# Optimization experiments

Measured on AMD Instinct MI355X. Metric: run time of the kernel, lower is better.

## Reference

```python
import jax, jax.numpy as jnp
import numpy as np

OBJECTNESS_LIMIT = 0.7
NUM_ANCHORS = 9
DN = ('NHWC', 'HWIO', 'NHWC')


def _conv(x, w, b):
    return jax.lax.conv_general_dilated(x, w, (1, 1), 'SAME', dimension_numbers=DN) + b


def setup_inputs() -> dict:
    key = jax.random.key(0)
    ks = jax.random.split(key, 4)
    B, H, W, Cin = 4, 256, 256, 64
    x = jax.random.normal(ks[0], (B, H, W, Cin), dtype=jnp.float32)
    # base: Conv2D(512, 3x3, relu, kernel_initializer='normal')
    w_base = jax.random.normal(ks[1], (3, 3, Cin, 512), dtype=jnp.float32) * 0.02
    b_base = jnp.zeros((512,), dtype=jnp.float32)
    # classifier: Conv2D(9, 1x1, sigmoid, kernel_initializer='uniform')
    w_cls = jax.random.uniform(ks[2], (1, 1, 512, NUM_ANCHORS), dtype=jnp.float32, minval=-0.05, maxval=0.05)
    b_cls = jnp.zeros((NUM_ANCHORS,), dtype=jnp.float32)
    w_reg = jax.random.normal(ks[3], (1, 1, 512, 4 * NUM_ANCHORS), dtype=jnp.float32) * 0.02
    b_reg = jnp.zeros((4 * NUM_ANCHORS,), dtype=jnp.float32)
    return {"x": x, "w_base": w_base, "b_base": b_base,
            "w_cls": w_cls, "b_cls": b_cls, "w_reg": w_reg, "b_reg": b_reg}


def reference(x, w_base, b_base, w_cls, b_cls, w_reg, b_reg):
    # shared 3x3 conv trunk
    feat = jax.nn.relu(_conv(x, w_base, b_base))                 # [B,H,W,512]
    # per-anchor objectness
    scores = jax.nn.sigmoid(_conv(feat, w_cls, b_cls))           # [B,H,W,A]
    deltas = _conv(feat, w_reg, b_reg)                           # [B,H,W,4A]
    B, H, W, A = scores.shape
    # vectorized form of the per-anchor threshold loop: keep deltas only
    # where objectness > limit (gather/filter expressed as a mask)
    mask = (scores > OBJECTNESS_LIMIT).astype(deltas.dtype)      # [B,H,W,A]
    masked = (deltas.reshape(B, H, W, A, 4) * mask[..., None]).reshape(B, H, W, 4 * A)
    return jnp.concatenate([scores, masked], axis=-1)            # [B,H,W,5A]
```

## Files before the change

kernel.cpp:

```cpp
#include <hip/hip_runtime.h>
#include <hip/hip_bf16.h>
#include <math.h>


typedef _Float16 fp16x8 __attribute__((ext_vector_type(8)));
typedef _Float16 fp16x4 __attribute__((ext_vector_type(4)));
typedef float    f32x4  __attribute__((ext_vector_type(4)));

#define BT_ELEMS  (18 * 32 * 64 * 8)
#define BT2_ELEMS (48 * 512)
#define BS_BYTES  32768

__global__ __launch_bounds__(256) void rpn_prep(
    const float* __restrict__ wb,
    const float* __restrict__ wc,
    const float* __restrict__ wr,
    _Float16* __restrict__ btI,
    _Float16* __restrict__ bt2_hi, _Float16* __restrict__ bt2_lo)
{
    int t = blockIdx.x * 256 + threadIdx.x;
    if (t < BT_ELEMS) {
        int e    = t & 7;
        int lane = (t >> 3) & 63;
        int j    = (t >> 9) & 31;
        int s    = t >> 14;
        int wv   = j >> 3, l = j & 7;
        int lr   = lane & 15, q = lane >> 4;
        int n    = wv * 128 + l * 16 + lr;
        int k    = s * 32 + q * 8 + e;
        int tap  = k >> 6, c = k & 63;
        btI[t] = (_Float16)wb[(tap * 64 + c) * 512 + n];
    } else if (t < BT_ELEMS + BT2_ELEMS) {
        int jj = t - BT_ELEMS;
        int k = jj & 511;
        int o = jj >> 9;
        float v = 0.f;
        if (o < 9)       v = wc[k * 9 + o];
        else if (o < 45) v = wr[k * 36 + (o - 9)];
        _Float16 h = (_Float16)v;
        bt2_hi[jj] = h;
        bt2_lo[jj] = (_Float16)(v - (float)h);
    }
}

#define XS_STRIDE   76
#define FB_OFF      10944
#define FB_PER_WAVE 4608
#define ZB_SLICE    1600
#define ARENA_BYTES 29376

#define LOAD_AH(S, AH)                                                        \
    {                                                                         \
        const int tap_ = (S) >> 1;                                            \
        const int ky_  = tap_ / 3;                                            \
        const int kx_  = tap_ - ky_ * 3;                                      \
        const int c0_  = ((S) & 1) * 32 + q * 8;                              \
        _Pragma("unroll")                                                     \
        for (int km = 0; km < 2; ++km)                                        \
            AH[km] = *(const fp16x8*)&xs_hi[((km + ky_) * 18 + lr + kx_) * XS_STRIDE + c0_]; \
    }

#define MFMA_STEP(AH, BREG)                                                   \
    {                                                                         \
        __builtin_amdgcn_s_setprio(1);                                        \
        _Pragma("unroll")                                                     \
        for (int l = 0; l < 8; ++l) {                                         \
            acc[0][l] = __builtin_amdgcn_mfma_f32_16x16x32_f16(AH[0], BREG[l], acc[0][l], 0, 0, 0); \
            acc[1][l] = __builtin_amdgcn_mfma_f32_16x16x32_f16(AH[1], BREG[l], acc[1][l], 0, 0, 0); \
        }                                                                     \
        __builtin_amdgcn_s_setprio(0);                                        \
    }

__global__ __launch_bounds__(256, 3) void rpn_main(
    const float* __restrict__ x,
    const float* __restrict__ b_base,
    const float* __restrict__ b_cls,
    const float* __restrict__ b_reg,
    const _Float16* __restrict__ btI,
    const _Float16* __restrict__ bt2_hi, const _Float16* __restrict__ bt2_lo,
    float* __restrict__ out)
{
    __shared__ char smem[ARENA_BYTES];
    _Float16* xs_hi = (_Float16*)smem;
    float*    zb    = (float*)smem;

    const int tid  = threadIdx.x;
    const int wave = tid >> 6;
    const int lane = tid & 63;
    const int q    = lane >> 4;
    const int lr   = lane & 15;
    const int n0   = wave * 128;

    const int wg  = blockIdx.x;
    const int b   = wg >> 11;
    const int rem = wg & 2047;
    const int h0  = (rem >> 4) * 2;
    const int w0  = (rem & 15) * 16;

    for (int i = 0; i < 5; ++i) {
        int flat = tid + i * 256;
        if (flat < 4 * 18 * 16) {
            int cq  = flat & 15;
            int rp  = flat >> 4;
            int row = rp / 18;
            int pos = rp - row * 18;
            int hh  = h0 - 1 + row;
            int ww  = w0 - 1 + pos;
            fp16x4 h4;
            if (hh >= 0 && hh < 256 && ww >= 0 && ww < 256) {
                const float4 v = *(const float4*)&x[(((b * 256 + hh) * 256 + ww) * 64 + cq * 4)];
                h4[0] = (_Float16)v.x; h4[1] = (_Float16)v.y;
                h4[2] = (_Float16)v.z; h4[3] = (_Float16)v.w;
            } else {
                #pragma unroll
                for (int j = 0; j < 4; ++j) h4[j] = (_Float16)0.f;
            }
            *(fp16x4*)&xs_hi[(row * 18 + pos) * XS_STRIDE + cq * 4] = h4;
        }
    }

    const char* gW = (const char*)btI + wave * 8192 + lane * 16;

    fp16x8 bA[8], bB[8];
    #pragma unroll
    for (int l = 0; l < 8; ++l)
        bA[l] = *(const fp16x8*)(gW + (size_t)l * 1024);

    __syncthreads();

    f32x4 acc[2][8];
    #pragma unroll
    for (int km = 0; km < 2; ++km)
        #pragma unroll
        for (int l = 0; l < 8; ++l)
            acc[km][l] = (f32x4){0.f, 0.f, 0.f, 0.f};

    fp16x8 ahA[2], ahB[2];
    LOAD_AH(0, ahA);

    #pragma unroll
    for (int s = 0; s < 18; s += 2) {
        {
            const char* g1 = gW + (size_t)(s + 1) * BS_BYTES;
            #pragma unroll
            for (int l = 0; l < 8; ++l)
                bB[l] = *(const fp16x8*)(g1 + (size_t)l * 1024);
        }
        LOAD_AH(s + 1, ahB);
        MFMA_STEP(ahA, bA);
        if (s + 2 < 18) {
            const char* g2 = gW + (size_t)(s + 2) * BS_BYTES;
            #pragma unroll
            for (int l = 0; l < 8; ++l)
                bA[l] = *(const fp16x8*)(g2 + (size_t)l * 1024);
            LOAD_AH(s + 2, ahA);
        }
        MFMA_STEP(ahB, bB);
    }


    _Float16* fh = (_Float16*)(smem + FB_OFF + wave * FB_PER_WAVE);
    _Float16* fl = fh + 32 * 36;

    f32x4 acc2[2][3];
    #pragma unroll
    for (int km = 0; km < 2; ++km)
        #pragma unroll
        for (int ns = 0; ns < 3; ++ns)
            acc2[km][ns] = (f32x4){0.f, 0.f, 0.f, 0.f};

    fp16x8 cwh0, cwl0, cwh1, cwh2;
    {
        const int kg0 = n0 + q * 8;
        cwh0 = *(const fp16x8*)&bt2_hi[(0 * 16 + lr) * 512 + kg0];
        cwl0 = *(const fp16x8*)&bt2_lo[(0 * 16 + lr) * 512 + kg0];
        cwh1 = *(const fp16x8*)&bt2_hi[(1 * 16 + lr) * 512 + kg0];
        cwh2 = *(const fp16x8*)&bt2_hi[(2 * 16 + lr) * 512 + kg0];
    }

    #pragma unroll
    for (int sub = 0; sub < 4; ++sub) {
        #pragma unroll
        for (int lh = 0; lh < 2; ++lh) {
            int l = sub * 2 + lh;
            float bias = b_base[n0 + l * 16 + lr];
            #pragma unroll
            for (int km = 0; km < 2; ++km) {
                #pragma unroll
                for (int r = 0; r < 4; ++r) {
                    float v = acc[km][l][r] + bias;
                    v = v > 0.f ? v : 0.f;
                    _Float16 h = (_Float16)v;
                    int row = km * 16 + q * 4 + r;
                    int col = lh * 16 + lr;
                    fh[row * 36 + col] = h;
                    fl[row * 36 + col] = (_Float16)(v - (float)h);
                }
            }
        }

        fp16x8 nwh0, nwl0, nwh1, nwh2;
        if (sub < 3) {
            const int kgn = n0 + (sub + 1) * 32 + q * 8;
            nwh0 = *(const fp16x8*)&bt2_hi[(0 * 16 + lr) * 512 + kgn];
            nwl0 = *(const fp16x8*)&bt2_lo[(0 * 16 + lr) * 512 + kgn];
            nwh1 = *(const fp16x8*)&bt2_hi[(1 * 16 + lr) * 512 + kgn];
            nwh2 = *(const fp16x8*)&bt2_hi[(2 * 16 + lr) * 512 + kgn];
        }

        asm volatile("s_waitcnt lgkmcnt(0)" ::: "memory");

        fp16x8 fah[2], fal[2];
        #pragma unroll
        for (int km = 0; km < 2; ++km) {
            int off = (km * 16 + lr) * 36 + q * 8;
            union { fp16x8 v8; fp16x4 v4[2]; } uh, ul;
            uh.v4[0] = *(const fp16x4*)&fh[off];
            uh.v4[1] = *(const fp16x4*)&fh[off + 4];
            ul.v4[0] = *(const fp16x4*)&fl[off];
            ul.v4[1] = *(const fp16x4*)&fl[off + 4];
            fah[km] = uh.v8;
            fal[km] = ul.v8;
        }

        __builtin_amdgcn_s_setprio(1);
        #pragma unroll
        for (int km = 0; km < 2; ++km)
            acc2[km][0] = __builtin_amdgcn_mfma_f32_16x16x32_f16(fah[km], cwh0, acc2[km][0], 0, 0, 0);
        #pragma unroll
        for (int km = 0; km < 2; ++km)
            acc2[km][0] = __builtin_amdgcn_mfma_f32_16x16x32_f16(fah[km], cwl0, acc2[km][0], 0, 0, 0);
        #pragma unroll
        for (int km = 0; km < 2; ++km)
            acc2[km][0] = __builtin_amdgcn_mfma_f32_16x16x32_f16(fal[km], cwh0, acc2[km][0], 0, 0, 0);
        #pragma unroll
        for (int km = 0; km < 2; ++km)
            acc2[km][1] = __builtin_amdgcn_mfma_f32_16x16x32_f16(fah[km], cwh1, acc2[km][1], 0, 0, 0);
        #pragma unroll
        for (int km = 0; km < 2; ++km)
            acc2[km][1] = __builtin_amdgcn_mfma_f32_16x16x32_f16(fal[km], cwh1, acc2[km][1], 0, 0, 0);
        #pragma unroll
        for (int km = 0; km < 2; ++km)
            acc2[km][2] = __builtin_amdgcn_mfma_f32_16x16x32_f16(fah[km], cwh2, acc2[km][2], 0, 0, 0);
        #pragma unroll
        for (int km = 0; km < 2; ++km)
            acc2[km][2] = __builtin_amdgcn_mfma_f32_16x16x32_f16(fal[km], cwh2, acc2[km][2], 0, 0, 0);
        __builtin_amdgcn_s_setprio(0);

        if (sub < 3) { cwh0 = nwh0; cwl0 = nwl0; cwh1 = nwh1; cwh2 = nwh2; }
    }

    __syncthreads();

    {
        float* zw = zb + wave * ZB_SLICE;
        #pragma unroll
        for (int km = 0; km < 2; ++km)
            #pragma unroll
            for (int ns = 0; ns < 3; ++ns)
                #pragma unroll
                for (int r = 0; r < 4; ++r) {
                    int row = km * 16 + q * 4 + r;
                    int col = ns * 16 + lr;
                    zw[row * 50 + col] = acc2[km][ns][r];
                }
    }
    __syncthreads();

    for (int i = tid; i < 32 * 45; i += 256) {
        int m = i / 45;
        int o = i - m * 45;
        int e0 = m * 50 + o;
        float z = ((zb[e0] + zb[ZB_SLICE + e0]) + zb[2 * ZB_SLICE + e0]) + zb[3 * ZB_SLICE + e0];
        float v;
        if (o < 9) {
            v = 1.f / (1.f + expf(-(z + b_cls[o])));
        } else {
            int d = o - 9;
            int a = d >> 2;
            int ea = m * 50 + a;
            float za = ((zb[ea] + zb[ZB_SLICE + ea]) + zb[2 * ZB_SLICE + ea]) + zb[3 * ZB_SLICE + ea];
            float s = 1.f / (1.f + expf(-(za + b_cls[a])));
            v = (s > 0.7f) ? (z + b_reg[d]) : 0.f;
        }
        int mh = m >> 4, mw = m & 15;
        out[(((b * 256 + h0 + mh) * 256) + w0 + mw) * 45 + o] = v;
    }
}

extern "C" void kernel_launch(void* const* d_in, const int* in_sizes, int n_in,
                              void* d_out, int out_size, void* d_ws, size_t ws_size,
                              hipStream_t stream)
{
    const float* x      = (const float*)d_in[0];
    const float* w_base = (const float*)d_in[1];
    const float* b_base = (const float*)d_in[2];
    const float* w_cls  = (const float*)d_in[3];
    const float* b_cls  = (const float*)d_in[4];
    const float* w_reg  = (const float*)d_in[5];
    const float* b_reg  = (const float*)d_in[6];
    float* out = (float*)d_out;

    _Float16* btI    = (_Float16*)d_ws;
    _Float16* bt2_hi = btI + BT_ELEMS;
    _Float16* bt2_lo = bt2_hi + BT2_ELEMS;

    rpn_prep<<<(BT_ELEMS + BT2_ELEMS + 255) / 256, 256, 0, stream>>>(
        w_base, w_cls, w_reg, btI, bt2_hi, bt2_lo);
    rpn_main<<<8192, 256, 0, stream>>>(
        x, b_base, b_cls, b_reg, btI, bt2_hi, bt2_lo, out);
}
```

Baseline: 346.9 us.

## Switch trunk conv MFMA from 16x16x32 to 32x32x16 tiles

Replaces the sixteen 16x16x32 MFMAs per K-step with eight 32x32x16 MFMAs covering the same 32x128 output tile per wave. The weight prep kernel re-packs the B operand into the 32x32 operand layout, the A fragments from LDS are reloaded to match, and the epilogue remaps the 16-element accumulators back to row/column positions. The aim is fewer MFMA issues and operand register reads per FLOP. The risk is that the remapped layouts or LDS access patterns create bank conflicts or pipeline stalls.

After: 368.8 us. 1.06x slower.

```diff
diff --git a/kernel.cpp b/kernel.cpp
--- a/kernel.cpp
+++ b/kernel.cpp
@@ -6,6 +6,7 @@
 typedef _Float16 fp16x8 __attribute__((ext_vector_type(8)));
 typedef _Float16 fp16x4 __attribute__((ext_vector_type(4)));
 typedef float    f32x4  __attribute__((ext_vector_type(4)));
+typedef float    f32x16 __attribute__((ext_vector_type(16)));
 
 #define BT_ELEMS  (18 * 32 * 64 * 8)
 #define BT2_ELEMS (48 * 512)
@@ -22,12 +23,12 @@
     if (t < BT_ELEMS) {
         int e    = t & 7;
         int lane = (t >> 3) & 63;
-        int j    = (t >> 9) & 31;
+        int j    = (t >> 9) & 3;
+        int h    = (t >> 11) & 1;
+        int wv   = (t >> 12) & 3;
         int s    = t >> 14;
-        int wv   = j >> 3, l = j & 7;
-        int lr   = lane & 15, q = lane >> 4;
-        int n    = wv * 128 + l * 16 + lr;
-        int k    = s * 32 + q * 8 + e;
+        int n    = wv * 128 + j * 32 + (lane & 31);
+        int k    = s * 32 + h * 16 + ((lane >> 5) << 3) + e;
         int tap  = k >> 6, c = k & 63;
         btI[t] = (_Float16)wb[(tap * 64 + c) * 512 + n];
     } else if (t < BT_ELEMS + BT2_ELEMS) {
@@ -54,20 +55,21 @@
         const int tap_ = (S) >> 1;                                            \
         const int ky_  = tap_ / 3;                                            \
         const int kx_  = tap_ - ky_ * 3;                                      \
-        const int c0_  = ((S) & 1) * 32 + q * 8;                              \
         _Pragma("unroll")                                                     \
-        for (int km = 0; km < 2; ++km)                                        \
-            AH[km] = *(const fp16x8*)&xs_hi[((km + ky_) * 18 + lr + kx_) * XS_STRIDE + c0_]; \
+        for (int h = 0; h < 2; ++h)                                           \
+            AH[h] = *(const fp16x8*)&xs_hi[((hp + ky_) * 18 + lr + kx_) * XS_STRIDE \
+                                           + ((S) & 1) * 32 + h * 16 + l5 * 8]; \
     }
 
 #define MFMA_STEP(AH, BREG)                                                   \
     {                                                                         \
         __builtin_amdgcn_s_setprio(1);                                        \
         _Pragma("unroll")                                                     \
-        for (int l = 0; l < 8; ++l) {                                         \
-            acc[0][l] = __builtin_amdgcn_mfma_f32_16x16x32_f16(AH[0], BREG[l], acc[0][l], 0, 0, 0); \
-            acc[1][l] = __builtin_amdgcn_mfma_f32_16x16x32_f16(AH[1], BREG[l], acc[1][l], 0, 0, 0); \
-        }                                                                     \
+        for (int j = 0; j < 4; ++j)                                           \
+            acc32[j] = __builtin_amdgcn_mfma_f32_32x32x16_f16(AH[0], BREG[j], acc32[j], 0, 0, 0); \
+        _Pragma("unroll")                                                     \
+        for (int j = 0; j < 4; ++j)                                           \
+            acc32[j] = __builtin_amdgcn_mfma_f32_32x32x16_f16(AH[1], BREG[4 + j], acc32[j], 0, 0, 0); \
         __builtin_amdgcn_s_setprio(0);                                        \
     }
 
@@ -89,6 +91,9 @@
     const int lane = tid & 63;
     const int q    = lane >> 4;
     const int lr   = lane & 15;
+    const int l5   = lane >> 5;
+    const int hp   = (lane >> 4) & 1;
+    const int l31  = lane & 31;
     const int n0   = wave * 128;
 
     const int wg  = blockIdx.x;
@@ -113,7 +118,7 @@
                 h4[2] = (_Float16)v.z; h4[3] = (_Float16)v.w;
             } else {
                 #pragma unroll
-                for (int j = 0; j < 4; ++j) h4[j] = (_Float16)0.f;
+                for (int jz = 0; jz < 4; ++jz) h4[jz] = (_Float16)0.f;
             }
             *(fp16x4*)&xs_hi[(row * 18 + pos) * XS_STRIDE + cq * 4] = h4;
         }
@@ -128,12 +133,12 @@
 
     __syncthreads();
 
-    f32x4 acc[2][8];
-    #pragma unroll
-    for (int km = 0; km < 2; ++km)
-        #pragma unroll
-        for (int l = 0; l < 8; ++l)
-            acc[km][l] = (f32x4){0.f, 0.f, 0.f, 0.f};
+    f32x16 acc32[4];
+    #pragma unroll
+    for (int j = 0; j < 4; ++j)
+        #pragma unroll
+        for (int r = 0; r < 16; ++r)
+            acc32[j][r] = 0.f;
 
     fp16x8 ahA[2], ahB[2];
     LOAD_AH(0, ahA);
@@ -180,22 +185,16 @@
 
     #pragma unroll
     for (int sub = 0; sub < 4; ++sub) {
-        #pragma unroll
-        for (int lh = 0; lh < 2; ++lh) {
-            int l = sub * 2 + lh;
-            float bias = b_base[n0 + l * 16 + lr];
+        {
+            float bias = b_base[n0 + sub * 32 + l31];
             #pragma unroll
-            for (int km = 0; km < 2; ++km) {
-                #pragma unroll
-                for (int r = 0; r < 4; ++r) {
-                    float v = acc[km][l][r] + bias;
-                    v = v > 0.f ? v : 0.f;
-                    _Float16 h = (_Float16)v;
-                    int row = km * 16 + q * 4 + r;
-                    int col = lh * 16 + lr;
-                    fh[row * 36 + col] = h;
-                    fl[row * 36 + col] = (_Float16)(v - (float)h);
-                }
+            for (int r = 0; r < 16; ++r) {
+                float v = acc32[sub][r] + bias;
+                v = v > 0.f ? v : 0.f;
+                _Float16 hh = (_Float16)v;
+                int m = (r & 3) + 8 * (r >> 2) + 4 * l5;
+                fh[m * 36 + l31] = hh;
+                fl[m * 36 + l31] = (_Float16)(v - (float)hh);
             }
         }
 
```
